# Kernel optimization log

Measured on AMD Instinct MI355X. Metric: run time of the kernel, lower is better.

## Reference

```python
import jax, jax.numpy as jnp
import numpy as np

B, S, E, H, C = 64, 512, 768, 768, 9
Q_GCE = 0.7
TAU = 0.7
IGNORE = -100


def setup_inputs() -> dict:
    key = jax.random.key(0)
    k_h, k_w1, k_w2, k_lab, k_drop = jax.random.split(key, 5)
    hidden = jax.random.normal(k_h, (B, S, E), dtype=jnp.float32)
    W1 = jax.random.normal(k_w1, (E, H), dtype=jnp.float32) * (1.0 / np.sqrt(E))
    b1 = jnp.zeros((H,), dtype=jnp.float32)
    W2 = jax.random.normal(k_w2, (H, C), dtype=jnp.float32) * (1.0 / np.sqrt(H))
    b2 = jnp.zeros((C,), dtype=jnp.float32)
    labels = jax.random.randint(k_lab, (B, S), 0, C, dtype=jnp.int64 if jax.config.jax_enable_x64 else jnp.int32)
    drop = jax.random.uniform(k_drop, (B, S)) < 0.1
    labels = jnp.where(drop, IGNORE, labels)
    return {"hidden": hidden, "W1": W1, "b1": b1, "W2": W2, "b2": b2,
            "labels": labels, "epoch": 5}


def reference(hidden, W1, b1, W2, b2, labels, epoch):
    # head: Linear -> Tanh -> Linear (dropout is identity at eval)
    h = jnp.tanh(jnp.einsum('bse,eh->bsh', hidden, W1) + b1)
    logit = jnp.einsum('bsh,hc->bsc', h, W2) + b2
    probs = jax.nn.softmax(logit, axis=2)  # [B,S,C]

    mask = labels != IGNORE
    safe_labels = jnp.where(mask, labels, 0)
    # p_i = probs[i, labels[i]] gathered for every token
    p = jnp.take_along_axis(probs, safe_labels[..., None], axis=2)[..., 0]  # [B,S]
    # GCE weight: w=1 for epoch<=2, else 1 if p>tau else 0 (constant wrt grads)
    w = jnp.where(epoch <= 2, 1.0, jnp.where(p > TAU, 1.0, 0.0))
    w = jax.lax.stop_gradient(w) * mask.astype(probs.dtype)
    loss = jnp.sum(w * (1.0 - jnp.power(p, Q_GCE)) / Q_GCE)
    return probs, loss
```

## Files before the change

kernel.cpp:

```cpp
#include <hip/hip_runtime.h>
#include <hip/hip_bf16.h>
#include <stdint.h>

#define E_ 768
#define H_ 768
#define C_ 9
#define M_TOTAL 32768
#define BM_ 64

typedef __attribute__((ext_vector_type(8))) __bf16 bf16x8;
typedef __attribute__((ext_vector_type(4))) float f32x4;
typedef __attribute__((ext_vector_type(4))) int i32x4;

static_assert(sizeof(bf16x8) == 16, "bf16x8 must be 16B");

__device__ __forceinline__ unsigned short f2bf(float f) {
    __hip_bfloat16 h = __float2bfloat16(f);
    return __builtin_bit_cast(unsigned short, h);
}

__global__ void prep_kernel(const float* __restrict__ W1, const float* __restrict__ W2,
                            unsigned short* __restrict__ W1f, unsigned short* __restrict__ W2f,
                            float* __restrict__ loss_out)
{
    int b = blockIdx.x;
    int n = threadIdx.x;
    if (b < 768) {
        int k = b;
        float v = W1[k * H_ + n];
        int ntile = n >> 4;
        int t = k >> 5;
        int lane = (n & 15) + 16 * ((k >> 3) & 3);
        int j = k & 7;
        W1f[((ntile * 24 + t) * 64 + lane) * 8 + j] = f2bf(v);
    } else {
        for (int it = 0; it < 16; ++it) {
            int tid = it * 768 + n;
            int j    = tid & 7;
            int lane = (tid >> 3) & 63;
            int t    = tid >> 9;
            int cls  = lane & 15;
            int k = t * 32 + (lane >> 4) * 8 + j;
            W2f[tid] = (cls < C_) ? f2bf(W2[k * C_ + cls]) : (unsigned short)0;
        }
        if (n == 0) *loss_out = 0.0f;
    }
}

__launch_bounds__(1024, 4)
__global__ void fused_head_kernel(const float* __restrict__ hidden,
                                  const unsigned short* __restrict__ W1f,
                                  const float* __restrict__ b1,
                                  const unsigned short* __restrict__ W2f,
                                  const float* __restrict__ b2,
                                  const int* __restrict__ labels,
                                  const int* __restrict__ epoch_p,
                                  float* __restrict__ probs,
                                  float* __restrict__ loss)
{
    __shared__ unsigned short Ash[24 * 4 * 512];

    const int tid  = threadIdx.x;
    const int w    = tid >> 6;
    const int lane = tid & 63;
    const int tok0 = blockIdx.x * BM_;
    const int c16  = lane & 15;
    const int q    = lane >> 4;

    const f32x4* hsrc = (const f32x4*)(hidden + (size_t)tok0 * E_);
    const int tkA = tid >> 5;
    const int fq  = tid & 31;
    const int t_l = fq >> 3;
    const int jj  = (fq & 1) * 4;
    const int q2s = (fq >> 1) & 3;

    f32x4 rg0, rg1;
    auto issue = [&](int c) {
        rg0 = __builtin_nontemporal_load(hsrc + (size_t)tkA * 192 + c * 32 + fq);
        rg1 = __builtin_nontemporal_load(hsrc + (size_t)(tkA + 32) * 192 + c * 32 + fq);
    };
    auto stage = [&](int bsel) {
        unsigned short* bufp = &Ash[bsel * 8192];
        {
            int lnf = (tkA & 15) + 16 * q2s;
            int mt  = tkA >> 4;
            ushort4 pk = { f2bf(rg0[0]), f2bf(rg0[1]), f2bf(rg0[2]), f2bf(rg0[3]) };
            *(ushort4*)(&bufp[((t_l * 4 + mt) * 64 + lnf) * 8 + jj]) = pk;
        }
        {
            int tk  = tkA + 32;
            int lnf = (tk & 15) + 16 * q2s;
            int mt  = tk >> 4;
            ushort4 pk = { f2bf(rg1[0]), f2bf(rg1[1]), f2bf(rg1[2]), f2bf(rg1[3]) };
            *(ushort4*)(&bufp[((t_l * 4 + mt) * 64 + lnf) * 8 + jj]) = pk;
        }
    };

    issue(0);

    const unsigned short* Wp = W1f + (size_t)(w * 3 * 24) * 512 + lane * 8;
    bf16x8 b0[3], b1v_[3];
    #pragma unroll
    for (int i = 0; i < 3; ++i)
        b0[i] = __builtin_bit_cast(bf16x8, *(const i32x4*)(Wp + (i * 24 + 0) * 512));
    #pragma unroll
    for (int i = 0; i < 3; ++i)
        b1v_[i] = __builtin_bit_cast(bf16x8, *(const i32x4*)(Wp + (i * 24 + 1) * 512));

    const f32x4 zero4 = {0.0f, 0.0f, 0.0f, 0.0f};
    f32x4 acc[4][3];
    #pragma unroll
    for (int mt = 0; mt < 4; ++mt)
        #pragma unroll
        for (int nt = 0; nt < 3; ++nt) acc[mt][nt] = zero4;

    stage(0);
    asm volatile("s_waitcnt lgkmcnt(0)\ns_barrier" ::: "memory");

    bf16x8 af[2][4];
    {
        const unsigned short* bufp = &Ash[0];
        #pragma unroll
        for (int mt = 0; mt < 4; ++mt)
            af[0][mt] = __builtin_bit_cast(bf16x8,
                *(const i32x4*)(&bufp[((0 * 4 + mt) * 64 + lane) * 8]));
    }

    #pragma unroll
    for (int c = 0; c < 6; ++c) {
        const unsigned short* bufp = &Ash[(c & 1) * 8192];
        if (c < 5) issue(c + 1);
        #pragma unroll
        for (int tl = 0; tl < 4; ++tl) {
            const int tt = 4 * c + tl;
            const int cur = tl & 1;
            if (tl < 3) {
                #pragma unroll
                for (int mt = 0; mt < 4; ++mt)
                    af[cur ^ 1][mt] = __builtin_bit_cast(bf16x8,
                        *(const i32x4*)(&bufp[(((tl + 1) * 4 + mt) * 64 + lane) * 8]));
            }
            __builtin_amdgcn_s_setprio(1);
            if ((tt & 1) == 0) {
                #pragma unroll
                for (int mt = 0; mt < 4; ++mt)
                    #pragma unroll
                    for (int nt = 0; nt < 3; ++nt)
                        acc[mt][nt] = __builtin_amdgcn_mfma_f32_16x16x32_bf16(
                            af[cur][mt], b0[nt], acc[mt][nt], 0, 0, 0);
            } else {
                #pragma unroll
                for (int mt = 0; mt < 4; ++mt)
                    #pragma unroll
                    for (int nt = 0; nt < 3; ++nt)
                        acc[mt][nt] = __builtin_amdgcn_mfma_f32_16x16x32_bf16(
                            af[cur][mt], b1v_[nt], acc[mt][nt], 0, 0, 0);
            }
            __builtin_amdgcn_s_setprio(0);
            if (tt + 2 < 24) {
                if ((tt & 1) == 0) {
                    #pragma unroll
                    for (int i = 0; i < 3; ++i)
                        b0[i] = __builtin_bit_cast(bf16x8,
                            *(const i32x4*)(Wp + (i * 24 + tt + 2) * 512));
                } else {
                    #pragma unroll
                    for (int i = 0; i < 3; ++i)
                        b1v_[i] = __builtin_bit_cast(bf16x8,
                            *(const i32x4*)(Wp + (i * 24 + tt + 2) * 512));
                }
            }
            if (tl == 1 && c < 5) stage((c + 1) & 1);
        }
        asm volatile("s_waitcnt lgkmcnt(0)\ns_barrier" ::: "memory");
        if (c < 5) {
            const unsigned short* bufn = &Ash[((c + 1) & 1) * 8192];
            #pragma unroll
            for (int mt = 0; mt < 4; ++mt)
                af[0][mt] = __builtin_bit_cast(bf16x8,
                    *(const i32x4*)(&bufn[((0 * 4 + mt) * 64 + lane) * 8]));
        }
    }

    unsigned short* Hsh = &Ash[0];
    #pragma unroll
    for (int i = 0; i < 3; ++i) {
        int col = w * 48 + i * 16 + c16;
        float b1b = b1[col];
        int t2 = col >> 5;
        int q2 = (col >> 3) & 3;
        int j  = col & 7;
        #pragma unroll
        for (int mt = 0; mt < 4; ++mt) {
            #pragma unroll
            for (int r = 0; r < 4; ++r) {
                float z = acc[mt][i][r] + b1b;
                float e = exp2f(z * 2.8853900817779268f);
                float th = 1.0f - 2.0f * __builtin_amdgcn_rcpf(e + 1.0f);
                int lanep = (q * 4 + r) + 16 * q2;
                Hsh[((t2 * 4 + mt) * 64 + lanep) * 8 + j] = f2bf(th);
            }
        }
    }
    asm volatile("s_waitcnt lgkmcnt(0)\ns_barrier" ::: "memory");

    if (w < 4) {
        f32x4 logit = zero4;
        #pragma unroll
        for (int t2 = 0; t2 < 24; ++t2) {
            bf16x8 ha = __builtin_bit_cast(bf16x8, *(const i32x4*)(&Hsh[((t2 * 4 + w) * 64 + lane) * 8]));
            bf16x8 wb = __builtin_bit_cast(bf16x8, *(const i32x4*)(W2f + ((size_t)t2 * 64 + lane) * 8));
            logit = __builtin_amdgcn_mfma_f32_16x16x32_bf16(ha, wb, logit, 0, 0, 0);
        }

        const bool valid = (c16 < C_);
        const float b2v = valid ? b2[c16] : 0.0f;
        const int ep = epoch_p[0];
        float lsum = 0.0f;
        #pragma unroll
        for (int r = 0; r < 4; ++r) {
            float l = valid ? (logit[r] + b2v) : -3.0e38f;
            float m = l;
            #pragma unroll
            for (int d = 1; d < 16; d <<= 1)
                m = fmaxf(m, __shfl_xor(m, d, 64));
            float e = valid ? exp2f((l - m) * 1.44269504f) : 0.0f;
            float s = e;
            #pragma unroll
            for (int d = 1; d < 16; d <<= 1)
                s += __shfl_xor(s, d, 64);
            float p = e / s;
            int row = tok0 + w * 16 + q * 4 + r;
            if (valid) __builtin_nontemporal_store(p, &probs[(size_t)row * C_ + c16]);
            int lab = labels[row];
            if (valid && lab == c16) {
                float wgt = (ep <= 2) ? 1.0f : ((p > 0.7f) ? 1.0f : 0.0f);
                if (wgt > 0.0f)
                    lsum += (1.0f - exp2f(0.7f * log2f(p))) * (1.0f / 0.7f);
            }
        }
        #pragma unroll
        for (int d = 1; d < 64; d <<= 1)
            lsum += __shfl_xor(lsum, d, 64);
        if (lane == 0) atomicAdd(loss, lsum);
    }
}

extern "C" void kernel_launch(void* const* d_in, const int* in_sizes, int n_in,
                              void* d_out, int out_size, void* d_ws, size_t ws_size,
                              hipStream_t stream)
{
    const float* hidden = (const float*)d_in[0];
    const float* W1     = (const float*)d_in[1];
    const float* b1     = (const float*)d_in[2];
    const float* W2     = (const float*)d_in[3];
    const float* b2     = (const float*)d_in[4];
    const int*   labels = (const int*)d_in[5];
    const int*   epoch  = (const int*)d_in[6];

    float* probs = (float*)d_out;
    float* loss  = probs + (size_t)M_TOTAL * C_;

    unsigned short* W1f = (unsigned short*)d_ws;
    unsigned short* W2f = W1f + 48 * 24 * 512;

    prep_kernel<<<769, 768, 0, stream>>>(W1, W2, W1f, W2f, loss);
    fused_head_kernel<<<M_TOTAL / BM_, 1024, 0, stream>>>(hidden, W1f, b1, W2f, b2,
                                                          labels, epoch, probs, loss);
}
```

Before: 214.6 us.

## Halve token tile to 32 with 8 waves each covering 96 output columns

Shrinks the per-block token tile from 64 to 32 and the block from 16 to 8 waves. Each wave now computes a 2x6 tile of MFMAs, so it covers 96 hidden columns instead of 48. The W1 fragment prefetch changes from double-buffered two steps ahead to a single register set reloaded one step ahead. The goal is more blocks, better load balance and a larger per-wave MFMA tile to reuse A fragments. The cost is twice as many W1 reads from L2 across blocks and less latency hiding on the weight loads.

```diff
diff --git a/kernel.cpp b/kernel.cpp
--- a/kernel.cpp
+++ b/kernel.cpp
@@ -6,7 +6,7 @@
 #define H_ 768
 #define C_ 9
 #define M_TOTAL 32768
-#define BM_ 64
+#define BM_ 32
 
 typedef __attribute__((ext_vector_type(8))) __bf16 bf16x8;
 typedef __attribute__((ext_vector_type(4))) float f32x4;
@@ -47,7 +47,7 @@
     }
 }
 
-__launch_bounds__(1024, 4)
+__launch_bounds__(512, 4)
 __global__ void fused_head_kernel(const float* __restrict__ hidden,
                                   const unsigned short* __restrict__ W1f,
                                   const float* __restrict__ b1,
@@ -58,7 +58,7 @@
                                   float* __restrict__ probs,
                                   float* __restrict__ loss)
 {
-    __shared__ unsigned short Ash[24 * 4 * 512];
+    __shared__ unsigned short Ash[24 * 2 * 512];
 
     const int tid  = threadIdx.x;
     const int w    = tid >> 6;
@@ -68,67 +68,62 @@
     const int q    = lane >> 4;
 
     const f32x4* hsrc = (const f32x4*)(hidden + (size_t)tok0 * E_);
-    const int tkA = tid >> 5;
-    const int fq  = tid & 31;
-    const int t_l = fq >> 3;
-    const int jj  = (fq & 1) * 4;
-    const int q2s = (fq >> 1) & 3;
-
-    f32x4 rg0, rg1;
+    const int tkA = tid >> 4;
+    const int fx  = tid & 15;
+    const int mtS = tkA >> 4;
+    const int tA_0 = fx >> 3,        tA_1 = (fx + 16) >> 3;
+    const int jj_0 = (fx & 1) * 4,   jj_1 = jj_0;
+    const int q2_0 = (fx >> 1) & 3,  q2_1 = ((fx + 16) >> 1) & 3;
+    const int lnf_0 = (tkA & 15) + 16 * q2_0;
+    const int lnf_1 = (tkA & 15) + 16 * q2_1;
+
+    f32x4 rgA, rgB;
     auto issue = [&](int c) {
-        rg0 = __builtin_nontemporal_load(hsrc + (size_t)tkA * 192 + c * 32 + fq);
-        rg1 = __builtin_nontemporal_load(hsrc + (size_t)(tkA + 32) * 192 + c * 32 + fq);
+        rgA = __builtin_nontemporal_load(hsrc + (size_t)tkA * 192 + c * 32 + fx);
+        rgB = __builtin_nontemporal_load(hsrc + (size_t)tkA * 192 + c * 32 + fx + 16);
     };
     auto stage = [&](int bsel) {
-        unsigned short* bufp = &Ash[bsel * 8192];
+        unsigned short* bufp = &Ash[bsel * 4096];
         {
-            int lnf = (tkA & 15) + 16 * q2s;
-            int mt  = tkA >> 4;
-            ushort4 pk = { f2bf(rg0[0]), f2bf(rg0[1]), f2bf(rg0[2]), f2bf(rg0[3]) };
-            *(ushort4*)(&bufp[((t_l * 4 + mt) * 64 + lnf) * 8 + jj]) = pk;
+            ushort4 pk = { f2bf(rgA[0]), f2bf(rgA[1]), f2bf(rgA[2]), f2bf(rgA[3]) };
+            *(ushort4*)(&bufp[((tA_0 * 2 + mtS) * 64 + lnf_0) * 8 + jj_0]) = pk;
         }
         {
-            int tk  = tkA + 32;
-            int lnf = (tk & 15) + 16 * q2s;
-            int mt  = tk >> 4;
-            ushort4 pk = { f2bf(rg1[0]), f2bf(rg1[1]), f2bf(rg1[2]), f2bf(rg1[3]) };
-            *(ushort4*)(&bufp[((t_l * 4 + mt) * 64 + lnf) * 8 + jj]) = pk;
+            ushort4 pk = { f2bf(rgB[0]), f2bf(rgB[1]), f2bf(rgB[2]), f2bf(rgB[3]) };
+            *(ushort4*)(&bufp[((tA_1 * 2 + mtS) * 64 + lnf_1) * 8 + jj_1]) = pk;
         }
     };
 
     issue(0);
 
-    const unsigned short* Wp = W1f + (size_t)(w * 3 * 24) * 512 + lane * 8;
-    bf16x8 b0[3], b1v_[3];
-    #pragma unroll
-    for (int i = 0; i < 3; ++i)
-        b0[i] = __builtin_bit_cast(bf16x8, *(const i32x4*)(Wp + (i * 24 + 0) * 512));
-    #pragma unroll
-    for (int i = 0; i < 3; ++i)
-        b1v_[i] = __builtin_bit_cast(bf16x8, *(const i32x4*)(Wp + (i * 24 + 1) * 512));
+    const unsigned short* Wp = W1f + (size_t)(w * 6 * 24) * 512 + lane * 8;
+    bf16x8 bF[6];
+    #pragma unroll
+    for (int i = 0; i < 6; ++i)
+        bF[i] = __builtin_bit_cast(bf16x8, *(const i32x4*)(Wp + (i * 24 + 0) * 512));
 
     const f32x4 zero4 = {0.0f, 0.0f, 0.0f, 0.0f};
-    f32x4 acc[4][3];
-    #pragma unroll
-    for (int mt = 0; mt < 4; ++mt)
-        #pragma unroll
-        for (int nt = 0; nt < 3; ++nt) acc[mt][nt] = zero4;
+    f32x4 acc[2][6];
+    #pragma unroll
+    for (int mt = 0; mt < 2; ++mt)
+        #pragma unroll
+        for (int nt = 0; nt < 6; ++nt) acc[mt][nt] = zero4;
 
     stage(0);
     asm volatile("s_waitcnt lgkmcnt(0)\ns_barrier" ::: "memory");
 
-    bf16x8 af[2][4];
+    bf16x8 af[2][2];
     {
         const unsigned short* bufp = &Ash[0];
         #pragma unroll
-        for (int mt = 0; mt < 4; ++mt)
+        for (int mt = 0; mt < 2; ++mt)
             af[0][mt] = __builtin_bit_cast(bf16x8,
-                *(const i32x4*)(&bufp[((0 * 4 + mt) * 64 + lane) * 8]));
+                *(const i32x4*)(&bufp[((0 * 2 + mt) * 64 + lane) * 8]));
     }
 
     #pragma unroll
     for (int c = 0; c < 6; ++c) {
-        const unsigned short* bufp = &Ash[(c & 1) * 8192];
+        const unsigned short* bufp = &Ash[(c & 1) * 4096];
         if (c < 5) issue(c + 1);
         #pragma unroll
         for (int tl = 0; tl < 4; ++tl) {
@@ -136,79 +131,63 @@
             const int cur = tl & 1;
             if (tl < 3) {
                 #pragma unroll
-                for (int mt = 0; mt < 4; ++mt)
+                for (int mt = 0; mt < 2; ++mt)
                     af[cur ^ 1][mt] = __builtin_bit_cast(bf16x8,
-                        *(const i32x4*)(&bufp[(((tl + 1) * 4 + mt) * 64 + lane) * 8]));
+                        *(const i32x4*)(&bufp[(((tl + 1) * 2 + mt) * 64 + lane) * 8]));
             }
             __builtin_amdgcn_s_setprio(1);
-            if ((tt & 1) == 0) {
+            #pragma unroll
+            for (int mt = 0; mt < 2; ++mt)
                 #pragma unroll
-                for (int mt = 0; mt < 4; ++mt)
-                    #pragma unroll
-                    for (int nt = 0; nt < 3; ++nt)
-                        acc[mt][nt] = __builtin_amdgcn_mfma_f32_16x16x32_bf16(
-                            af[cur][mt], b0[nt], acc[mt][nt], 0, 0, 0);
-            } else {
+                for (int nt = 0; nt < 6; ++nt)
+                    acc[mt][nt] = __builtin_amdgcn_mfma_f32_16x16x32_bf16(
+                        af[cur][mt], bF[nt], acc[mt][nt], 0, 0, 0);
+            __builtin_amdgcn_s_setprio(0);
+            if (tt + 1 < 24) {
                 #pragma unroll
-                for (int mt = 0; mt < 4; ++mt)
-                    #pragma unroll
-                    for (int nt = 0; nt < 3; ++nt)
-                        acc[mt][nt] = __builtin_amdgcn_mfma_f32_16x16x32_bf16(
-                            af[cur][mt], b1v_[nt], acc[mt][nt], 0, 0, 0);
-            }
-            __builtin_amdgcn_s_setprio(0);
-            if (tt + 2 < 24) {
-                if ((tt & 1) == 0) {
-                    #pragma unroll
-                    for (int i = 0; i < 3; ++i)
-                        b0[i] = __builtin_bit_cast(bf16x8,
-                            *(const i32x4*)(Wp + (i * 24 + tt + 2) * 512));
-                } else {
-                    #pragma unroll
-                    for (int i = 0; i < 3; ++i)
-                        b1v_[i] = __builtin_bit_cast(bf16x8,
-                            *(const i32x4*)(Wp + (i * 24 + tt + 2) * 512));
-                }
+                for (int i = 0; i < 6; ++i)
+                    bF[i] = __builtin_bit_cast(bf16x8,
+                        *(const i32x4*)(Wp + (i * 24 + tt + 1) * 512));
             }
             if (tl == 1 && c < 5) stage((c + 1) & 1);
         }
         asm volatile("s_waitcnt lgkmcnt(0)\ns_barrier" ::: "memory");
         if (c < 5) {
-            const unsigned short* bufn = &Ash[((c + 1) & 1) * 8192];
-            #pragma unroll
-            for (int mt = 0; mt < 4; ++mt)
+            const unsigned short* bufn = &Ash[((c + 1) & 1) * 4096];
+            #pragma unroll
+            for (int mt = 0; mt < 2; ++mt)
                 af[0][mt] = __builtin_bit_cast(bf16x8,
-                    *(const i32x4*)(&bufn[((0 * 4 + mt) * 64 + lane) * 8]));
+                    *(const i32x4*)(&bufn[((0 * 2 + mt) * 64 + lane) * 8]));
         }
     }
 
     unsigned short* Hsh = &Ash[0];
     #pragma unroll
-    for (int i = 0; i < 3; ++i) {
-        int col = w * 48 + i * 16 + c16;
+    for (int i = 0; i < 6; ++i) {
+        int col = (w * 6 + i) * 16 + c16;
         float b1b = b1[col];
         int t2 = col >> 5;
         int q2 = (col >> 3) & 3;
         int j  = col & 7;
         #pragma unroll
-        for (int mt = 0; mt < 4; ++mt) {
+        for (int mt = 0; mt < 2; ++mt) {
             #pragma unroll
             for (int r = 0; r < 4; ++r) {
                 float z = acc[mt][i][r] + b1b;
                 float e = exp2f(z * 2.8853900817779268f);
                 float th = 1.0f - 2.0f * __builtin_amdgcn_rcpf(e + 1.0f);
                 int lanep = (q * 4 + r) + 16 * q2;
-                Hsh[((t2 * 4 + mt) * 64 + lanep) * 8 + j] = f2bf(th);
+                Hsh[((t2 * 2 + mt) * 64 + lanep) * 8 + j] = f2bf(th);
             }
         }
     }
     asm volatile("s_waitcnt lgkmcnt(0)\ns_barrier" ::: "memory");
 
-    if (w < 4) {
+    if (w < 2) {
         f32x4 logit = zero4;
         #pragma unroll
         for (int t2 = 0; t2 < 24; ++t2) {
-            bf16x8 ha = __builtin_bit_cast(bf16x8, *(const i32x4*)(&Hsh[((t2 * 4 + w) * 64 + lane) * 8]));
+            bf16x8 ha = __builtin_bit_cast(bf16x8, *(const i32x4*)(&Hsh[((t2 * 2 + w) * 64 + lane) * 8]));
             bf16x8 wb = __builtin_bit_cast(bf16x8, *(const i32x4*)(W2f + ((size_t)t2 * 64 + lane) * 8));
             logit = __builtin_amdgcn_mfma_f32_16x16x32_bf16(ha, wb, logit, 0, 0, 0);
         }
@@ -265,6 +244,6 @@
     unsigned short* W2f = W1f + 48 * 24 * 512;
 
     prep_kernel<<<769, 768, 0, stream>>>(W1, W2, W1f, W2f, loss);
-    fused_head_kernel<<<M_TOTAL / BM_, 1024, 0, stream>>>(hidden, W1f, b1, W2f, b2,
-                                                          labels, epoch, probs, loss);
-}
+    fused_head_kernel<<<M_TOTAL / BM_, 512, 0, stream>>>(hidden, W1f, b1, W2f, b2,
+                                                         labels, epoch, probs, loss);
+}
```

After: 212.8 us. About the same (-0.9%).

## Stream W1 tiles into LDS via async global_load_lds double buffering

Applied to the files above, without the earlier changes.

Replaces the per-wave register prefetch of W1 fragments from global memory with asynchronous global-to-LDS direct loads into a double-buffered LDS region, synchronized with explicit vmcnt waits. LDS grows to 128KB to hold two W1 k-slices plus the A staging buffers. The goal is to cut VGPR pressure and global-load latency stalls in the MFMA loop. In exchange it adds LDS reads per k-step and much higher LDS use, which limits blocks per CU. There are also no barriers on the B buffers, but each wave reads only the cells it loaded itself.

```diff
diff --git a/kernel.cpp b/kernel.cpp
--- a/kernel.cpp
+++ b/kernel.cpp
@@ -11,6 +11,9 @@
 typedef __attribute__((ext_vector_type(8))) __bf16 bf16x8;
 typedef __attribute__((ext_vector_type(4))) float f32x4;
 typedef __attribute__((ext_vector_type(4))) int i32x4;
+
+#define GLOBAL_AS __attribute__((address_space(1)))
+#define LDS_AS    __attribute__((address_space(3)))
 
 static_assert(sizeof(bf16x8) == 16, "bf16x8 must be 16B");
 
@@ -58,7 +61,7 @@
                                   float* __restrict__ probs,
                                   float* __restrict__ loss)
 {
-    __shared__ unsigned short Ash[24 * 4 * 512];
+    __shared__ unsigned short L[65536];
 
     const int tid  = threadIdx.x;
     const int w    = tid >> 6;
@@ -80,7 +83,7 @@
         rg1 = __builtin_nontemporal_load(hsrc + (size_t)(tkA + 32) * 192 + c * 32 + fq);
     };
     auto stage = [&](int bsel) {
-        unsigned short* bufp = &Ash[bsel * 8192];
+        unsigned short* bufp = &L[49152 + bsel * 8192];
         {
             int lnf = (tkA & 15) + 16 * q2s;
             int mt  = tkA >> 4;
@@ -88,7 +91,7 @@
             *(ushort4*)(&bufp[((t_l * 4 + mt) * 64 + lnf) * 8 + jj]) = pk;
         }
         {
-            int tk  = tkA + 32;
+            int tk = tkA + 32;
             int lnf = (tk & 15) + 16 * q2s;
             int mt  = tk >> 4;
             ushort4 pk = { f2bf(rg1[0]), f2bf(rg1[1]), f2bf(rg1[2]), f2bf(rg1[3]) };
@@ -96,16 +99,21 @@
         }
     };
 
+    auto issueB = [&](int kk) {
+        const int bb = (kk & 1) * 24576;
+        #pragma unroll
+        for (int i = 0; i < 3; ++i) {
+            const int cell = w * 3 + i;
+            const unsigned short* g = W1f + ((size_t)(cell * 24 + kk) * 64 + lane) * 8;
+            __builtin_amdgcn_global_load_lds((const GLOBAL_AS void*)g,
+                                             (LDS_AS void*)&L[bb + cell * 512],
+                                             16, 0, 0);
+        }
+    };
+
     issue(0);
-
-    const unsigned short* Wp = W1f + (size_t)(w * 3 * 24) * 512 + lane * 8;
-    bf16x8 b0[3], b1v_[3];
-    #pragma unroll
-    for (int i = 0; i < 3; ++i)
-        b0[i] = __builtin_bit_cast(bf16x8, *(const i32x4*)(Wp + (i * 24 + 0) * 512));
-    #pragma unroll
-    for (int i = 0; i < 3; ++i)
-        b1v_[i] = __builtin_bit_cast(bf16x8, *(const i32x4*)(Wp + (i * 24 + 1) * 512));
+    issueB(0);
+    asm volatile("" ::: "memory");
 
     const f32x4 zero4 = {0.0f, 0.0f, 0.0f, 0.0f};
     f32x4 acc[4][3];
@@ -119,70 +127,61 @@
 
     bf16x8 af[2][4];
     {
-        const unsigned short* bufp = &Ash[0];
+        const unsigned short* abuf = &L[49152];
         #pragma unroll
         for (int mt = 0; mt < 4; ++mt)
             af[0][mt] = __builtin_bit_cast(bf16x8,
-                *(const i32x4*)(&bufp[((0 * 4 + mt) * 64 + lane) * 8]));
+                *(const i32x4*)(&abuf[((0 * 4 + mt) * 64 + lane) * 8]));
     }
 
     #pragma unroll
     for (int c = 0; c < 6; ++c) {
-        const unsigned short* bufp = &Ash[(c & 1) * 8192];
+        const unsigned short* abuf = &L[49152 + (c & 1) * 8192];
         if (c < 5) issue(c + 1);
+        asm volatile("" ::: "memory");
         #pragma unroll
         for (int tl = 0; tl < 4; ++tl) {
-            const int tt = 4 * c + tl;
+            const int k = 4 * c + tl;
             const int cur = tl & 1;
+            if (k + 1 < 24) issueB(k + 1);
+            if (tl == 0 && c < 5)      asm volatile("s_waitcnt vmcnt(5)" ::: "memory");
+            else if (k == 23)          asm volatile("s_waitcnt vmcnt(0)" ::: "memory");
+            else                       asm volatile("s_waitcnt vmcnt(3)" ::: "memory");
+            bf16x8 bf[3];
+            {
+                const unsigned short* bbuf = &L[(k & 1) * 24576];
+                #pragma unroll
+                for (int i = 0; i < 3; ++i)
+                    bf[i] = __builtin_bit_cast(bf16x8,
+                        *(const i32x4*)(&bbuf[(w * 3 + i) * 512 + lane * 8]));
+            }
             if (tl < 3) {
                 #pragma unroll
                 for (int mt = 0; mt < 4; ++mt)
                     af[cur ^ 1][mt] = __builtin_bit_cast(bf16x8,
-                        *(const i32x4*)(&bufp[(((tl + 1) * 4 + mt) * 64 + lane) * 8]));
+                        *(const i32x4*)(&abuf[(((tl + 1) * 4 + mt) * 64 + lane) * 8]));
             }
             __builtin_amdgcn_s_setprio(1);
-            if ((tt & 1) == 0) {
+            #pragma unroll
+            for (int mt = 0; mt < 4; ++mt)
                 #pragma unroll
-                for (int mt = 0; mt < 4; ++mt)
-                    #pragma unroll
-                    for (int nt = 0; nt < 3; ++nt)
-                        acc[mt][nt] = __builtin_amdgcn_mfma_f32_16x16x32_bf16(
-                            af[cur][mt], b0[nt], acc[mt][nt], 0, 0, 0);
-            } else {
-                #pragma unroll
-                for (int mt = 0; mt < 4; ++mt)
-                    #pragma unroll
-                    for (int nt = 0; nt < 3; ++nt)
-                        acc[mt][nt] = __builtin_amdgcn_mfma_f32_16x16x32_bf16(
-                            af[cur][mt], b1v_[nt], acc[mt][nt], 0, 0, 0);
-            }
+                for (int nt = 0; nt < 3; ++nt)
+                    acc[mt][nt] = __builtin_amdgcn_mfma_f32_16x16x32_bf16(
+                        af[cur][mt], bf[nt], acc[mt][nt], 0, 0, 0);
             __builtin_amdgcn_s_setprio(0);
-            if (tt + 2 < 24) {
-                if ((tt & 1) == 0) {
-                    #pragma unroll
-                    for (int i = 0; i < 3; ++i)
-                        b0[i] = __builtin_bit_cast(bf16x8,
-                            *(const i32x4*)(Wp + (i * 24 + tt + 2) * 512));
-                } else {
-                    #pragma unroll
-                    for (int i = 0; i < 3; ++i)
-                        b1v_[i] = __builtin_bit_cast(bf16x8,
-                            *(const i32x4*)(Wp + (i * 24 + tt + 2) * 512));
-                }
-            }
             if (tl == 1 && c < 5) stage((c + 1) & 1);
         }
         asm volatile("s_waitcnt lgkmcnt(0)\ns_barrier" ::: "memory");
         if (c < 5) {
-            const unsigned short* bufn = &Ash[((c + 1) & 1) * 8192];
+            const unsigned short* abn = &L[49152 + ((c + 1) & 1) * 8192];
             #pragma unroll
             for (int mt = 0; mt < 4; ++mt)
                 af[0][mt] = __builtin_bit_cast(bf16x8,
-                    *(const i32x4*)(&bufn[((0 * 4 + mt) * 64 + lane) * 8]));
-        }
-    }
-
-    unsigned short* Hsh = &Ash[0];
+                    *(const i32x4*)(&abn[((0 * 4 + mt) * 64 + lane) * 8]));
+        }
+    }
+
+    unsigned short* Hsh = &L[0];
     #pragma unroll
     for (int i = 0; i < 3; ++i) {
         int col = w * 48 + i * 16 + c16;
```

Result: slower. 227.7 us (+6.1%).

## Split hidden dimension across two blocks per tile with atomic logit reduction

Applied to the files above, without the earlier changes.

Each 64-token tile is now handled by two 512-thread blocks, each computing half of the 768 hidden columns and a partial second-layer logit. The partial logits are accumulated into a zeroed workspace with global atomics, and a per-tile counter picks the last-arriving block to run softmax, probs store and loss. This doubles the grid and halves block size to raise occupancy and parallelism. In exchange it re-reads hidden twice per tile, adds workspace zeroing in the prep kernel and atomic traffic, and relies on an acq_rel flag for visibility of the partial sums.

```diff
diff --git a/kernel.cpp b/kernel.cpp
--- a/kernel.cpp
+++ b/kernel.cpp
@@ -19,9 +19,11 @@
     return __builtin_bit_cast(unsigned short, h);
 }
 
+#define ZWORDS (524288 + 512)
+
 __global__ void prep_kernel(const float* __restrict__ W1, const float* __restrict__ W2,
                             unsigned short* __restrict__ W1f, unsigned short* __restrict__ W2f,
-                            float* __restrict__ loss_out)
+                            float* __restrict__ loss_out, unsigned int* __restrict__ zws)
 {
     int b = blockIdx.x;
     int n = threadIdx.x;
@@ -33,7 +35,7 @@
         int lane = (n & 15) + 16 * ((k >> 3) & 3);
         int j = k & 7;
         W1f[((ntile * 24 + t) * 64 + lane) * 8 + j] = f2bf(v);
-    } else {
+    } else if (b == 768) {
         for (int it = 0; it < 16; ++it) {
             int tid = it * 768 + n;
             int j    = tid & 7;
@@ -44,10 +46,14 @@
             W2f[tid] = (cls < C_) ? f2bf(W2[k * C_ + cls]) : (unsigned short)0;
         }
         if (n == 0) *loss_out = 0.0f;
-    }
-}
-
-__launch_bounds__(1024, 4)
+    } else {
+        size_t base = (size_t)(b - 769) * 1024;
+        if (base + n < ZWORDS) zws[base + n] = 0u;
+        if (n < 256 && base + 768 + n < ZWORDS) zws[base + 768 + n] = 0u;
+    }
+}
+
+__launch_bounds__(512, 4)
 __global__ void fused_head_kernel(const float* __restrict__ hidden,
                                   const unsigned short* __restrict__ W1f,
                                   const float* __restrict__ b1,
@@ -56,49 +62,48 @@
                                   const int* __restrict__ labels,
                                   const int* __restrict__ epoch_p,
                                   float* __restrict__ probs,
-                                  float* __restrict__ loss)
+                                  float* __restrict__ loss,
+                                  float* __restrict__ Lws,
+                                  int* __restrict__ flags)
 {
-    __shared__ unsigned short Ash[24 * 4 * 512];
+    __shared__ unsigned short Ash[24576];
+    __shared__ int finFlag;
 
     const int tid  = threadIdx.x;
     const int w    = tid >> 6;
     const int lane = tid & 63;
-    const int tok0 = blockIdx.x * BM_;
+    const int tile = blockIdx.x >> 1;
+    const int half = blockIdx.x & 1;
+    const int tok0 = tile * BM_;
     const int c16  = lane & 15;
     const int q    = lane >> 4;
 
     const f32x4* hsrc = (const f32x4*)(hidden + (size_t)tok0 * E_);
-    const int tkA = tid >> 5;
-    const int fq  = tid & 31;
-    const int t_l = fq >> 3;
-    const int jj  = (fq & 1) * 4;
-    const int q2s = (fq >> 1) & 3;
-
-    f32x4 rg0, rg1;
+    f32x4 rg[4];
     auto issue = [&](int c) {
-        rg0 = __builtin_nontemporal_load(hsrc + (size_t)tkA * 192 + c * 32 + fq);
-        rg1 = __builtin_nontemporal_load(hsrc + (size_t)(tkA + 32) * 192 + c * 32 + fq);
+        #pragma unroll
+        for (int i = 0; i < 4; ++i) {
+            int slot = i * 512 + tid;
+            int tk = slot >> 5, fq = slot & 31;
+            rg[i] = __builtin_nontemporal_load(hsrc + (size_t)tk * 192 + c * 32 + fq);
+        }
     };
     auto stage = [&](int bsel) {
         unsigned short* bufp = &Ash[bsel * 8192];
-        {
-            int lnf = (tkA & 15) + 16 * q2s;
-            int mt  = tkA >> 4;
-            ushort4 pk = { f2bf(rg0[0]), f2bf(rg0[1]), f2bf(rg0[2]), f2bf(rg0[3]) };
+        #pragma unroll
+        for (int i = 0; i < 4; ++i) {
+            int slot = i * 512 + tid;
+            int tk = slot >> 5, fq = slot & 31;
+            int t_l = fq >> 3, jj = (fq & 1) * 4, q2s = (fq >> 1) & 3;
+            int lnf = (tk & 15) + 16 * q2s, mt = tk >> 4;
+            ushort4 pk = { f2bf(rg[i][0]), f2bf(rg[i][1]), f2bf(rg[i][2]), f2bf(rg[i][3]) };
             *(ushort4*)(&bufp[((t_l * 4 + mt) * 64 + lnf) * 8 + jj]) = pk;
         }
-        {
-            int tk  = tkA + 32;
-            int lnf = (tk & 15) + 16 * q2s;
-            int mt  = tk >> 4;
-            ushort4 pk = { f2bf(rg1[0]), f2bf(rg1[1]), f2bf(rg1[2]), f2bf(rg1[3]) };
-            *(ushort4*)(&bufp[((t_l * 4 + mt) * 64 + lnf) * 8 + jj]) = pk;
-        }
     };
 
     issue(0);
 
-    const unsigned short* Wp = W1f + (size_t)(w * 3 * 24) * 512 + lane * 8;
+    const unsigned short* Wp = W1f + (size_t)(half * 24 + w * 3) * 24 * 512 + lane * 8;
     bf16x8 b0[3], b1v_[3];
     #pragma unroll
     for (int i = 0; i < 3; ++i)
@@ -185,11 +190,11 @@
     unsigned short* Hsh = &Ash[0];
     #pragma unroll
     for (int i = 0; i < 3; ++i) {
-        int col = w * 48 + i * 16 + c16;
-        float b1b = b1[col];
-        int t2 = col >> 5;
-        int q2 = (col >> 3) & 3;
-        int j  = col & 7;
+        int colL = w * 48 + i * 16 + c16;
+        float b1b = b1[half * 384 + colL];
+        int t2 = colL >> 5;
+        int q2 = (colL >> 3) & 3;
+        int j  = colL & 7;
         #pragma unroll
         for (int mt = 0; mt < 4; ++mt) {
             #pragma unroll
@@ -204,22 +209,44 @@
     }
     asm volatile("s_waitcnt lgkmcnt(0)\ns_barrier" ::: "memory");
 
+    f32x4 logit = zero4;
     if (w < 4) {
-        f32x4 logit = zero4;
-        #pragma unroll
-        for (int t2 = 0; t2 < 24; ++t2) {
+        #pragma unroll
+        for (int t2 = 0; t2 < 12; ++t2) {
             bf16x8 ha = __builtin_bit_cast(bf16x8, *(const i32x4*)(&Hsh[((t2 * 4 + w) * 64 + lane) * 8]));
-            bf16x8 wb = __builtin_bit_cast(bf16x8, *(const i32x4*)(W2f + ((size_t)t2 * 64 + lane) * 8));
+            bf16x8 wb = __builtin_bit_cast(bf16x8, *(const i32x4*)(W2f + ((size_t)(half * 12 + t2) * 64 + lane) * 8));
             logit = __builtin_amdgcn_mfma_f32_16x16x32_bf16(ha, wb, logit, 0, 0, 0);
         }
-
+        if (c16 < C_) {
+            #pragma unroll
+            for (int r = 0; r < 4; ++r) {
+                int row = tok0 + w * 16 + q * 4 + r;
+                __hip_atomic_fetch_add(&Lws[(size_t)row * 16 + c16], logit[r],
+                                       __ATOMIC_RELAXED, __HIP_MEMORY_SCOPE_AGENT);
+            }
+        }
+    }
+    __syncthreads();
+
+    if (tid == 0) {
+        finFlag = __hip_atomic_fetch_add(&flags[tile], 1,
+                                         __ATOMIC_ACQ_REL, __HIP_MEMORY_SCOPE_AGENT);
+    }
+    __syncthreads();
+
+    if (finFlag == 1 && w < 4) {
         const bool valid = (c16 < C_);
         const float b2v = valid ? b2[c16] : 0.0f;
         const int ep = epoch_p[0];
         float lsum = 0.0f;
         #pragma unroll
         for (int r = 0; r < 4; ++r) {
-            float l = valid ? (logit[r] + b2v) : -3.0e38f;
+            int row = tok0 + w * 16 + q * 4 + r;
+            float l = -3.0e38f;
+            if (valid) {
+                l = __hip_atomic_load(&Lws[(size_t)row * 16 + c16],
+                                      __ATOMIC_RELAXED, __HIP_MEMORY_SCOPE_AGENT) + b2v;
+            }
             float m = l;
             #pragma unroll
             for (int d = 1; d < 16; d <<= 1)
@@ -230,7 +257,6 @@
             for (int d = 1; d < 16; d <<= 1)
                 s += __shfl_xor(s, d, 64);
             float p = e / s;
-            int row = tok0 + w * 16 + q * 4 + r;
             if (valid) __builtin_nontemporal_store(p, &probs[(size_t)row * C_ + c16]);
             int lab = labels[row];
             if (valid && lab == c16) {
@@ -263,8 +289,11 @@
 
     unsigned short* W1f = (unsigned short*)d_ws;
     unsigned short* W2f = W1f + 48 * 24 * 512;
-
-    prep_kernel<<<769, 768, 0, stream>>>(W1, W2, W1f, W2f, loss);
-    fused_head_kernel<<<M_TOTAL / BM_, 1024, 0, stream>>>(hidden, W1f, b1, W2f, b2,
-                                                          labels, epoch, probs, loss);
-}
+    float* Lws   = (float*)(W2f + 24 * 512);
+    int*   flags = (int*)(Lws + 524288);
+
+    prep_kernel<<<1289, 768, 0, stream>>>(W1, W2, W1f, W2f, loss, (unsigned int*)Lws);
+    fused_head_kernel<<<(M_TOTAL / BM_) * 2, 512, 0, stream>>>(hidden, W1f, b1, W2f, b2,
+                                                               labels, epoch, probs, loss,
+                                                               Lws, flags);
+}
```

New measurement: 285.0 us. 1.33x slower.
